# Kernel optimization log

Hardware: AMD Instinct MI355X
Metric: run time of the kernel (lower is better)

## Reference

```python
import jax, jax.numpy as jnp
import numpy as np

B, S, D, H, DFF = 4, 1024, 1024, 16, 4096
MAX_LEN = 1024
DK = D // H
EPS = 1e-5


def _ln(x, g, b):
    m = jnp.mean(x, axis=-1, keepdims=True)
    v = jnp.mean(jnp.square(x - m), axis=-1, keepdims=True)
    return (x - m) / jnp.sqrt(v + EPS) * g + b


def setup_inputs() -> dict:
    key = jax.random.key(0)
    ks = jax.random.split(key, 16)
    s = 0.02
    inp = {
        "x": jax.random.normal(ks[0], (B, S, D), jnp.float32),
        "wq": jax.random.normal(ks[1], (D, D), jnp.float32) * s,
        "bq": jnp.zeros((D,), jnp.float32),
        "wk": jax.random.normal(ks[2], (D, D), jnp.float32) * s,
        "bk": jnp.zeros((D,), jnp.float32),
        "wv": jax.random.normal(ks[3], (D, D), jnp.float32) * s,
        "bv": jnp.zeros((D,), jnp.float32),
        "wo": jax.random.normal(ks[4], (D, D), jnp.float32) * s,
        "bo": jnp.zeros((D,), jnp.float32),
        "rel_table": jax.random.normal(ks[5], (2 * MAX_LEN - 1, H), jnp.float32) * s,
        "ln1_g": jnp.ones((D,), jnp.float32),
        "ln1_b": jnp.zeros((D,), jnp.float32),
        "w1": jax.random.normal(ks[6], (D, DFF), jnp.float32) * s,
        "b1": jnp.zeros((DFF,), jnp.float32),
        "w2": jax.random.normal(ks[7], (DFF, D), jnp.float32) * s,
        "b2": jnp.zeros((D,), jnp.float32),
        "ln2_g": jnp.ones((D,), jnp.float32),
        "ln2_b": jnp.zeros((D,), jnp.float32),
        "mask": jnp.ones((B, 1, 1, S), jnp.int32),
    }
    return inp


def reference(x, wq, bq, wk, bk, wv, bv, wo, bo, rel_table,
              ln1_g, ln1_b, w1, b1, w2, b2, ln2_g, ln2_b, mask):
    # --- multi-head attention with relative position bias (post-LN encoder layer, eval mode) ---
    q = (x @ wq + bq).reshape(B, S, H, DK).transpose(0, 2, 1, 3)  # [B,H,S,dk]
    k = (x @ wk + bk).reshape(B, S, H, DK).transpose(0, 2, 1, 3)
    v = (x @ wv + bv).reshape(B, S, H, DK).transpose(0, 2, 1, 3)

    scores = jnp.einsum('bhqd,bhkd->bhqk', q, k) / jnp.sqrt(jnp.float32(DK))

    # relative position bias: table[(q - k + max_len - 1).clip] -> [1,H,S,S]
    coords = jnp.arange(S)[:, None] - jnp.arange(S)[None, :] + (MAX_LEN - 1)
    coords = jnp.clip(coords, 0, 2 * MAX_LEN - 2)
    bias = rel_table[coords]              # [S,S,H]
    scores = scores + bias.transpose(2, 0, 1)[None]

    scores = jnp.where(mask == 0, jnp.float32(-1e9), scores)
    attn = jax.nn.softmax(scores, axis=-1)
    ctx = jnp.einsum('bhqk,bhkd->bhqd', attn, v)
    ctx = ctx.transpose(0, 2, 1, 3).reshape(B, S, D)
    attn_out = ctx @ wo + bo

    x1 = _ln(x + attn_out, ln1_g, ln1_b)

    ff = jax.nn.relu(x1 @ w1 + b1) @ w2 + b2
    return _ln(x1 + ff, ln2_g, ln2_b)
```

## Files before the change

kernel.cpp:

```cpp
#include <hip/hip_runtime.h>
#include <hip/hip_bf16.h>

typedef __hip_bfloat16 bf16;
typedef __attribute__((ext_vector_type(8))) short short8;
typedef __attribute__((ext_vector_type(4))) float f32x4;

#define LOG2E 1.4426950408889634f

typedef const __attribute__((address_space(1))) void* gptr_t;
typedef __attribute__((address_space(3))) void* sptr_t;

__device__ __forceinline__ void async16(void* lds, const void* g) {
  __builtin_amdgcn_global_load_lds((gptr_t)g, (sptr_t)lds, 16, 0, 0);
}

__device__ __forceinline__ float bf2f(unsigned short u) {
  union { unsigned int i; float f; } c; c.i = ((unsigned int)u) << 16; return c.f;
}


__global__ __launch_bounds__(256) void prep_all(
    const float* __restrict__ x, const float* __restrict__ bq,
    const float* __restrict__ bk, const float* __restrict__ bv,
    const float* __restrict__ wq, const float* __restrict__ wk,
    const float* __restrict__ wv, const float* __restrict__ wo,
    const float* __restrict__ w1, const float* __restrict__ w2,
    bf16* __restrict__ xb, float* __restrict__ bqkv,
    bf16* __restrict__ dqkv, bf16* __restrict__ dwo,
    bf16* __restrict__ dw1, bf16* __restrict__ dw2) {
  const int bid = blockIdx.x;
  if (bid < 4096) {
    int i = (bid * 256 + threadIdx.x) * 4;
    float4 v = *(const float4*)(x + i);
    bf16 h4[4] = {__float2bfloat16(v.x), __float2bfloat16(v.y),
                  __float2bfloat16(v.z), __float2bfloat16(v.w)};
    *(uint2*)((unsigned short*)xb + i) = *(uint2*)h4;
    return;
  }
  if (bid == 16384) {
#pragma unroll
    for (int j = 0; j < 12; ++j) {
      int i = j * 256 + threadIdx.x;
      bqkv[i] = (i < 1024) ? bq[i] : (i < 2048 ? bk[i - 1024] : bv[i - 2048]);
    }
    return;
  }
  __shared__ float tl[32][33];
  const int tid = bid - 4096;
  const float* s;
  bf16* d;
  int NN, KK, n0, k0;
  if (tid < 4096) {
    int m = tid >> 10, tile = tid & 1023;
    s = m == 0 ? wq : m == 1 ? wk : m == 2 ? wv : wo;
    d = m < 3 ? dqkv + (size_t)m * 1024 * 1024 : dwo;
    NN = 1024; KK = 1024;
    n0 = (tile & 31) * 32; k0 = (tile >> 5) * 32;
  } else if (tid < 8192) {
    int tile = tid - 4096;
    s = w1; d = dw1; NN = 4096; KK = 1024;
    n0 = (tile & 127) * 32; k0 = (tile >> 7) * 32;
  } else {
    int tile = tid - 8192;
    s = w2; d = dw2; NN = 1024; KK = 4096;
    n0 = (tile & 31) * 32; k0 = (tile >> 5) * 32;
  }
  const int tx = threadIdx.x & 31, ty = threadIdx.x >> 5;
#pragma unroll
  for (int j = 0; j < 4; ++j)
    tl[ty + j * 8][tx] = s[(size_t)(k0 + ty + j * 8) * NN + n0 + tx];
  __syncthreads();
#pragma unroll
  for (int j = 0; j < 4; ++j)
    d[(size_t)(n0 + ty + j * 8) * KK + k0 + tx] =
        __float2bfloat16(tl[tx][ty + j * 8]);
}


template <int RELU, int VT>
__global__ __launch_bounds__(256) void gemm_bt(
    const bf16* __restrict__ A, const bf16* __restrict__ Bt,
    const float* __restrict__ bias, bf16* __restrict__ C,
    bf16* __restrict__ vt, int M, int N, int K) {
  __shared__ bf16 As[2][128 * 64];
  __shared__ bf16 Bs[2][128 * 64];
  const int t = threadIdx.x;
  const int w = t >> 6, l = t & 63;
  const int m0 = blockIdx.x * 128, n0 = blockIdx.y * 128;
  const int wr = (w >> 1) * 64, wc = (w & 1) * 64;
  const int srow = l >> 3, scol = l & 7;
  const int lm = l & 15, lq = l >> 4;

  f32x4 acc[4][4];
#pragma unroll
  for (int i = 0; i < 4; ++i)
#pragma unroll
    for (int j = 0; j < 4; ++j) acc[i][j] = (f32x4){0.f, 0.f, 0.f, 0.f};

  auto stage = [&](int k0, int d) {
#pragma unroll
    for (int p = 0; p < 4; ++p) {
      int row = p * 32 + w * 8 + srow;
      int gc = scol ^ (row & 7);
      async16(&As[d][(p * 32 + w * 8) * 64], A + (size_t)(m0 + row) * K + k0 + gc * 8);
      async16(&Bs[d][(p * 32 + w * 8) * 64], Bt + (size_t)(n0 + row) * K + k0 + gc * 8);
    }
  };

  stage(0, 0);
  const int niter = K >> 6;
  for (int it = 0; it < niter; ++it) {
    const int d = it & 1;
    __syncthreads();
    short8 af[2][4], bfr[2][4];
#pragma unroll
    for (int kk = 0; kk < 2; ++kk)
#pragma unroll
      for (int mi = 0; mi < 4; ++mi) {
        int rowa = wr + mi * 16 + lm;
        af[kk][mi] = *(const short8*)&As[d][rowa * 64 + (((kk * 4 + lq) ^ (rowa & 7)) << 3)];
        int rowb = wc + mi * 16 + lm;
        bfr[kk][mi] = *(const short8*)&Bs[d][rowb * 64 + (((kk * 4 + lq) ^ (rowb & 7)) << 3)];
      }
    if (it + 1 < niter) stage((it + 1) << 6, d ^ 1);
#pragma unroll
    for (int kk = 0; kk < 2; ++kk)
#pragma unroll
      for (int mi = 0; mi < 4; ++mi)
#pragma unroll
        for (int ni = 0; ni < 4; ++ni)
          acc[mi][ni] = __builtin_amdgcn_mfma_f32_16x16x32_bf16(
              af[kk][mi], bfr[kk][ni], acc[mi][ni], 0, 0, 0);
  }

#pragma unroll
  for (int mi = 0; mi < 4; ++mi)
#pragma unroll
    for (int ni = 0; ni < 4; ++ni) {
      int col = n0 + wc + ni * 16 + lm;
      int row0 = m0 + wr + mi * 16 + lq * 4;
      float bv = bias[col];
      float v[4];
#pragma unroll
      for (int r = 0; r < 4; ++r) {
        v[r] = acc[mi][ni][r] + bv;
        if (RELU) v[r] = fmaxf(v[r], 0.f);
        C[(size_t)(row0 + r) * N + col] = __float2bfloat16(v[r]);
      }
      if (VT && col >= 2048) {
        int vcol = col - 2048;
        int bh = (row0 >> 10) * 16 + (vcol >> 6);
        int dk = vcol & 63;
        int s = row0 & 1023;
        bf16 h4[4] = {__float2bfloat16(v[0]), __float2bfloat16(v[1]),
                      __float2bfloat16(v[2]), __float2bfloat16(v[3])};
        *(uint2*)&vt[((size_t)bh * 64 + dk) * 1024 + s] = *(uint2*)h4;
      }
    }
}

__global__ __launch_bounds__(256) void gemm_bt_splitk(
    const bf16* __restrict__ A, const bf16* __restrict__ Bt,
    bf16* __restrict__ P, int M, int N, int lda, int KS) {
  __shared__ bf16 As[2][128 * 64];
  __shared__ bf16 Bs[2][128 * 64];
  const int t = threadIdx.x;
  const int w = t >> 6, l = t & 63;
  const int m0 = blockIdx.x * 128, n0 = blockIdx.y * 128;
  const int kstart = blockIdx.z * KS;
  const int wr = (w >> 1) * 64, wc = (w & 1) * 64;
  const int srow = l >> 3, scol = l & 7;
  const int lm = l & 15, lq = l >> 4;

  f32x4 acc[4][4];
#pragma unroll
  for (int i = 0; i < 4; ++i)
#pragma unroll
    for (int j = 0; j < 4; ++j) acc[i][j] = (f32x4){0.f, 0.f, 0.f, 0.f};

  auto stage = [&](int k0, int d) {
#pragma unroll
    for (int p = 0; p < 4; ++p) {
      int row = p * 32 + w * 8 + srow;
      int gc = scol ^ (row & 7);
      async16(&As[d][(p * 32 + w * 8) * 64], A + (size_t)(m0 + row) * lda + k0 + gc * 8);
      async16(&Bs[d][(p * 32 + w * 8) * 64], Bt + (size_t)(n0 + row) * lda + k0 + gc * 8);
    }
  };

  stage(kstart, 0);
  const int niter = KS >> 6;
  for (int it = 0; it < niter; ++it) {
    const int d = it & 1;
    __syncthreads();
    short8 af[2][4], bfr[2][4];
#pragma unroll
    for (int kk = 0; kk < 2; ++kk)
#pragma unroll
      for (int mi = 0; mi < 4; ++mi) {
        int rowa = wr + mi * 16 + lm;
        af[kk][mi] = *(const short8*)&As[d][rowa * 64 + (((kk * 4 + lq) ^ (rowa & 7)) << 3)];
        int rowb = wc + mi * 16 + lm;
        bfr[kk][mi] = *(const short8*)&Bs[d][rowb * 64 + (((kk * 4 + lq) ^ (rowb & 7)) << 3)];
      }
    if (it + 1 < niter) stage(kstart + ((it + 1) << 6), d ^ 1);
#pragma unroll
    for (int kk = 0; kk < 2; ++kk)
#pragma unroll
      for (int mi = 0; mi < 4; ++mi)
#pragma unroll
        for (int ni = 0; ni < 4; ++ni)
          acc[mi][ni] = __builtin_amdgcn_mfma_f32_16x16x32_bf16(
              af[kk][mi], bfr[kk][ni], acc[mi][ni], 0, 0, 0);
  }
  bf16* Pz = P + (size_t)blockIdx.z * M * N;
#pragma unroll
  for (int mi = 0; mi < 4; ++mi)
#pragma unroll
    for (int r = 0; r < 4; ++r) {
      int row = m0 + wr + mi * 16 + lq * 4 + r;
#pragma unroll
      for (int ni = 0; ni < 4; ++ni) {
        int col = n0 + wc + ni * 16 + lm;
        Pz[(size_t)row * N + col] = __float2bfloat16(acc[mi][ni][r]);
      }
    }
}


__global__ __launch_bounds__(512, 4) void flash_attn(
    const bf16* __restrict__ qkv, const bf16* __restrict__ vt,
    const float* __restrict__ rel, const int* __restrict__ mask,
    bf16* __restrict__ ctx) {
  __shared__ bf16 Kl[2][64 * 64];
  __shared__ bf16 Vl[2][64 * 64];
  __shared__ bf16 Pl[128 * 64];
  __shared__ float bias_s[2][192];
  __shared__ float mask_s[2][64];

  const int t = threadIdx.x;
  const int w = t >> 6, l = t & 63;
  const int lm = l & 15, lq = l >> 4;
  const int qt = blockIdx.x, bh = blockIdx.y;
  const int b = bh >> 4, h = bh & 15;
  const int q0 = qt * 128;
  const int srow = l >> 3;
  const int gc = (l & 7) ^ srow;
  const int qq = w * 16 + lm;

  auto stage = [&](int d, int k0n) {
    async16(&Kl[d][w * 8 * 64],
            qkv + (size_t)(b * 1024 + k0n + w * 8 + srow) * 3072 + 1024 + h * 64 + gc * 8);
    async16(&Vl[d][w * 8 * 64],
            vt + ((size_t)bh * 64 + w * 8 + srow) * 1024 + k0n + gc * 8);
    if (t < 191) bias_s[d][t] = rel[(q0 - k0n + 960 + t) * 16 + h] * LOG2E;
    if (t < 64) mask_s[d][t] = (mask[b * 1024 + k0n + t] == 0) ? -1.44e9f : 0.f;
  };

#pragma unroll
  for (int p = 0; p < 2; ++p)
    async16(&Pl[(p * 64 + w * 8) * 64],
            qkv + (size_t)(b * 1024 + q0 + p * 64 + w * 8 + srow) * 3072 + h * 64 + gc * 8);
  stage(0, 0);
  __syncthreads();

  short8 qf[2];
#pragma unroll
  for (int kk = 0; kk < 2; ++kk)
    qf[kk] = *(const short8*)&Pl[qq * 64 + (((kk * 4 + lq) ^ (lm & 7)) << 3)];
  __syncthreads();

  float l_acc = 0.f;
  f32x4 acc_o[4];
#pragma unroll
  for (int j = 0; j < 4; ++j) acc_o[j] = (f32x4){0.f, 0.f, 0.f, 0.f};

  const float C0 = 0.125f * LOG2E;

  for (int kt = 0; kt < 16; ++kt) {
    const int d = kt & 1;
    if (kt < 15) stage(d ^ 1, (kt + 1) * 64);

    f32x4 sa[4];
#pragma unroll
    for (int i = 0; i < 4; ++i) sa[i] = (f32x4){0.f, 0.f, 0.f, 0.f};
#pragma unroll
    for (int kk = 0; kk < 2; ++kk) {
      short8 ak[4];
#pragma unroll
      for (int mi = 0; mi < 4; ++mi) {
        int row = mi * 16 + lm;
        ak[mi] = *(const short8*)&Kl[d][row * 64 + (((kk * 4 + lq) ^ (lm & 7)) << 3)];
      }
#pragma unroll
      for (int mi = 0; mi < 4; ++mi)
        sa[mi] = __builtin_amdgcn_mfma_f32_16x16x32_bf16(ak[mi], qf[kk], sa[mi], 0, 0, 0);
    }

    float m4[4][4];
#pragma unroll
    for (int mi = 0; mi < 4; ++mi)
      *(float4*)m4[mi] = *(const float4*)&mask_s[d][mi * 16 + lq * 4];
#pragma unroll
    for (int mi = 0; mi < 4; ++mi)
#pragma unroll
      for (int r = 0; r < 4; ++r) {
        int kl = mi * 16 + lq * 4 + r;
        float p = __builtin_amdgcn_exp2f(
            fmaf(sa[mi][r], C0, bias_s[d][qq - kl + 63] + m4[mi][r]));
        sa[mi][r] = p;
        l_acc += p;
      }

#pragma unroll
    for (int mi = 0; mi < 4; ++mi) {
      bf16 h4[4];
#pragma unroll
      for (int r = 0; r < 4; ++r) h4[r] = __float2bfloat16(sa[mi][r]);
      int chunk = mi * 2 + (lq >> 1);
      *(uint2*)&Pl[qq * 64 + ((chunk ^ (lm & 7)) << 3) + ((lq & 1) << 2)] =
          *(uint2*)h4;
    }

#pragma unroll
    for (int kk2 = 0; kk2 < 2; ++kk2) {
      short8 pf = *(const short8*)&Pl[qq * 64 + (((kk2 * 4 + lq) ^ (lm & 7)) << 3)];
      short8 vf[4];
#pragma unroll
      for (int ni = 0; ni < 4; ++ni) {
        int rowv = ni * 16 + lm;
        vf[ni] = *(const short8*)&Vl[d][rowv * 64 + (((kk2 * 4 + lq) ^ (lm & 7)) << 3)];
      }
#pragma unroll
      for (int ni = 0; ni < 4; ++ni)
        acc_o[ni] = __builtin_amdgcn_mfma_f32_16x16x32_bf16(pf, vf[ni], acc_o[ni], 0, 0, 0);
    }
    __syncthreads();
  }

  l_acc += __shfl_xor(l_acc, 16);
  l_acc += __shfl_xor(l_acc, 32);
  float linv = 1.f / l_acc;
#pragma unroll
  for (int r = 0; r < 4; ++r) {
    float il = __shfl(linv, lq * 4 + r);
    int qx = w * 16 + lq * 4 + r;
    size_t rowbase = (size_t)(b * 1024 + q0 + qx) * 1024 + h * 64;
#pragma unroll
    for (int ni = 0; ni < 4; ++ni)
      ctx[rowbase + ni * 16 + lm] = __float2bfloat16(acc_o[ni][r] * il);
  }
}


template <int NS>
__global__ __launch_bounds__(256) void ln_resid(
    const float* __restrict__ xin, const bf16* __restrict__ part,
    const float* __restrict__ bias,
    const float* __restrict__ gw, const float* __restrict__ bw,
    float* __restrict__ outf, bf16* __restrict__ outb) {
  const int row = blockIdx.x, t = threadIdx.x;
  const size_t base = (size_t)row * 1024 + t * 4;
  float4 xv = *(const float4*)(xin + base);
  float4 bi = *(const float4*)(bias + t * 4);
  float v0 = xv.x + bi.x, v1 = xv.y + bi.y, v2 = xv.z + bi.z, v3 = xv.w + bi.w;
#pragma unroll
  for (int s = 0; s < NS; ++s) {
    const bf16* p = part + (size_t)s * 4194304 + base;
    ushort4 pv = *(const ushort4*)p;
    v0 += bf2f(pv.x); v1 += bf2f(pv.y); v2 += bf2f(pv.z); v3 += bf2f(pv.w);
  }
  float s1 = v0 + v1 + v2 + v3;
  float s2 = v0 * v0 + v1 * v1 + v2 * v2 + v3 * v3;
#pragma unroll
  for (int o = 1; o < 64; o <<= 1) {
    s1 += __shfl_xor(s1, o);
    s2 += __shfl_xor(s2, o);
  }
  __shared__ float red[8];
  const int w = t >> 6, l = t & 63;
  if (l == 0) { red[w] = s1; red[4 + w] = s2; }
  __syncthreads();
  float S1 = red[0] + red[1] + red[2] + red[3];
  float S2 = red[4] + red[5] + red[6] + red[7];
  float mean = S1 * (1.f / 1024.f);
  float var = S2 * (1.f / 1024.f) - mean * mean;
  float rstd = rsqrtf(var + 1e-5f);
  float4 gv = *(const float4*)(gw + t * 4);
  float4 bv = *(const float4*)(bw + t * 4);
  float o0 = (v0 - mean) * rstd * gv.x + bv.x;
  float o1 = (v1 - mean) * rstd * gv.y + bv.y;
  float o2 = (v2 - mean) * rstd * gv.z + bv.z;
  float o3 = (v3 - mean) * rstd * gv.w + bv.w;
  if (outf) {
    float4 ov = {o0, o1, o2, o3};
    *(float4*)(outf + base) = ov;
  }
  if (outb) {
    bf16 h4[4] = {__float2bfloat16(o0), __float2bfloat16(o1),
                  __float2bfloat16(o2), __float2bfloat16(o3)};
    *(uint2*)((unsigned short*)outb + base) = *(uint2*)h4;
  }
}


extern "C" void kernel_launch(void* const* d_in, const int* in_sizes, int n_in,
                              void* d_out, int out_size, void* d_ws, size_t ws_size,
                              hipStream_t stream) {
  (void)in_sizes; (void)n_in; (void)out_size; (void)ws_size;
  const float* x   = (const float*)d_in[0];
  const float* wq  = (const float*)d_in[1];
  const float* bq  = (const float*)d_in[2];
  const float* wk  = (const float*)d_in[3];
  const float* bk  = (const float*)d_in[4];
  const float* wv  = (const float*)d_in[5];
  const float* bv  = (const float*)d_in[6];
  const float* wo  = (const float*)d_in[7];
  const float* bo  = (const float*)d_in[8];
  const float* rel = (const float*)d_in[9];
  const float* g1  = (const float*)d_in[10];
  const float* be1 = (const float*)d_in[11];
  const float* w1  = (const float*)d_in[12];
  const float* b1  = (const float*)d_in[13];
  const float* w2  = (const float*)d_in[14];
  const float* b2  = (const float*)d_in[15];
  const float* g2  = (const float*)d_in[16];
  const float* be2 = (const float*)d_in[17];
  const int* mask  = (const int*)d_in[18];
  float* out = (float*)d_out;

  char* ws = (char*)d_ws;
  bf16*  xb      = (bf16*)(ws + 0);
  bf16*  wqkv_t  = (bf16*)(ws + 8388608);
  bf16*  wo_t    = (bf16*)(ws + 14680064);
  bf16*  w1_t    = (bf16*)(ws + 16777216);
  bf16*  ctx_b   = (bf16*)(ws + 25165824);
  bf16*  x1b     = (bf16*)(ws + 33554432);
  bf16*  qkv_b   = (bf16*)(ws + 41943040);
  bf16*  vtb     = (bf16*)(ws + 67108864);
  bf16*  part_wo = (bf16*)(ws + 41943040);
  bf16*  h1      = (bf16*)(ws + 41943040);
  bf16*  part_ff = (bf16*)(ws + 0);
  bf16*  w2_t    = (bf16*)(ws + 75497472);
  float* x1f     = (float*)(ws + 83886080);
  float* bqkv    = (float*)(ws + 100663296);

  prep_all<<<16385, 256, 0, stream>>>(x, bq, bk, bv, wq, wk, wv, wo, w1, w2,
                                      xb, bqkv, wqkv_t, wo_t, w1_t, w2_t);

  gemm_bt<0, 1><<<dim3(32, 24), 256, 0, stream>>>(
      xb, wqkv_t, bqkv, qkv_b, vtb, 4096, 3072, 1024);
  flash_attn<<<dim3(8, 64), 512, 0, stream>>>(qkv_b, vtb, rel, mask, ctx_b);
  gemm_bt_splitk<<<dim3(32, 8, 2), 256, 0, stream>>>(
      ctx_b, wo_t, part_wo, 4096, 1024, 1024, 512);
  ln_resid<2><<<4096, 256, 0, stream>>>(x, part_wo, bo, g1, be1, x1f, x1b);
  gemm_bt<1, 0><<<dim3(32, 32), 256, 0, stream>>>(
      x1b, w1_t, b1, h1, nullptr, 4096, 4096, 1024);
  gemm_bt_splitk<<<dim3(32, 8, 2), 256, 0, stream>>>(
      h1, w2_t, part_ff, 4096, 1024, 4096, 2048);
  ln_resid<2><<<4096, 256, 0, stream>>>(x1f, part_ff, b2, g2, be2, out, nullptr);
}
```

Baseline: 323.2 us.

## Halve flash-attention query tile and read bf16 residual in second LayerNorm

The attention kernel now uses 64-query tiles with 256 threads per block, doubling the grid to 16x64 blocks. Each wave loads two 8-row chunks of K and V, and the bias and Q staging buffers shrink to match. Separately, the second residual LayerNorm reads the bf16 copy of x1 instead of a separate fp32 copy, so the fp32 x1 write and its re-read are gone. In exchange, the smaller tile loads each K/V tile for fewer queries, so K/V traffic per query goes up, and using a bf16 residual lowers precision.

```diff
diff --git a/kernel.cpp b/kernel.cpp
--- a/kernel.cpp
+++ b/kernel.cpp
@@ -228,14 +228,14 @@
 }
 
 
-__global__ __launch_bounds__(512, 4) void flash_attn(
+__global__ __launch_bounds__(256, 3) void flash_attn(
     const bf16* __restrict__ qkv, const bf16* __restrict__ vt,
     const float* __restrict__ rel, const int* __restrict__ mask,
     bf16* __restrict__ ctx) {
   __shared__ bf16 Kl[2][64 * 64];
   __shared__ bf16 Vl[2][64 * 64];
-  __shared__ bf16 Pl[128 * 64];
-  __shared__ float bias_s[2][192];
+  __shared__ bf16 Pl[64 * 64];
+  __shared__ float bias_s[2][128];
   __shared__ float mask_s[2][64];
 
   const int t = threadIdx.x;
@@ -243,24 +243,30 @@
   const int lm = l & 15, lq = l >> 4;
   const int qt = blockIdx.x, bh = blockIdx.y;
   const int b = bh >> 4, h = bh & 15;
-  const int q0 = qt * 128;
+  const int q0 = qt * 64;
   const int srow = l >> 3;
   const int gc = (l & 7) ^ srow;
   const int qq = w * 16 + lm;
 
   auto stage = [&](int d, int k0n) {
-    async16(&Kl[d][w * 8 * 64],
-            qkv + (size_t)(b * 1024 + k0n + w * 8 + srow) * 3072 + 1024 + h * 64 + gc * 8);
-    async16(&Vl[d][w * 8 * 64],
-            vt + ((size_t)bh * 64 + w * 8 + srow) * 1024 + k0n + gc * 8);
-    if (t < 191) bias_s[d][t] = rel[(q0 - k0n + 960 + t) * 16 + h] * LOG2E;
+#pragma unroll
+    for (int p = 0; p < 2; ++p) {
+      int rbase = w * 16 + p * 8;
+      async16(&Kl[d][rbase * 64],
+              qkv + (size_t)(b * 1024 + k0n + rbase + srow) * 3072 + 1024 + h * 64 + gc * 8);
+      async16(&Vl[d][rbase * 64],
+              vt + ((size_t)bh * 64 + rbase + srow) * 1024 + k0n + gc * 8);
+    }
+    if (t < 127) bias_s[d][t] = rel[(q0 - k0n + 960 + t) * 16 + h] * LOG2E;
     if (t < 64) mask_s[d][t] = (mask[b * 1024 + k0n + t] == 0) ? -1.44e9f : 0.f;
   };
 
 #pragma unroll
-  for (int p = 0; p < 2; ++p)
-    async16(&Pl[(p * 64 + w * 8) * 64],
-            qkv + (size_t)(b * 1024 + q0 + p * 64 + w * 8 + srow) * 3072 + h * 64 + gc * 8);
+  for (int p = 0; p < 2; ++p) {
+    int rbase = w * 16 + p * 8;
+    async16(&Pl[rbase * 64],
+            qkv + (size_t)(b * 1024 + q0 + rbase + srow) * 3072 + h * 64 + gc * 8);
+  }
   stage(0, 0);
   __syncthreads();
 
@@ -353,17 +359,24 @@
 }
 
 
-template <int NS>
+template <typename RT, int NS>
 __global__ __launch_bounds__(256) void ln_resid(
-    const float* __restrict__ xin, const bf16* __restrict__ part,
+    const RT* __restrict__ xin, const bf16* __restrict__ part,
     const float* __restrict__ bias,
     const float* __restrict__ gw, const float* __restrict__ bw,
     float* __restrict__ outf, bf16* __restrict__ outb) {
   const int row = blockIdx.x, t = threadIdx.x;
   const size_t base = (size_t)row * 1024 + t * 4;
-  float4 xv = *(const float4*)(xin + base);
+  float v0, v1, v2, v3;
+  if constexpr (sizeof(RT) == 4) {
+    float4 xv = *(const float4*)(xin + base);
+    v0 = xv.x; v1 = xv.y; v2 = xv.z; v3 = xv.w;
+  } else {
+    ushort4 xv = *(const ushort4*)((const unsigned short*)xin + base);
+    v0 = bf2f(xv.x); v1 = bf2f(xv.y); v2 = bf2f(xv.z); v3 = bf2f(xv.w);
+  }
   float4 bi = *(const float4*)(bias + t * 4);
-  float v0 = xv.x + bi.x, v1 = xv.y + bi.y, v2 = xv.z + bi.z, v3 = xv.w + bi.w;
+  v0 += bi.x; v1 += bi.y; v2 += bi.z; v3 += bi.w;
 #pragma unroll
   for (int s = 0; s < NS; ++s) {
     const bf16* p = part + (size_t)s * 4194304 + base;
@@ -442,7 +455,6 @@
   bf16*  h1      = (bf16*)(ws + 41943040);
   bf16*  part_ff = (bf16*)(ws + 0);
   bf16*  w2_t    = (bf16*)(ws + 75497472);
-  float* x1f     = (float*)(ws + 83886080);
   float* bqkv    = (float*)(ws + 100663296);
 
   prep_all<<<16385, 256, 0, stream>>>(x, bq, bk, bv, wq, wk, wv, wo, w1, w2,
@@ -450,13 +462,13 @@
 
   gemm_bt<0, 1><<<dim3(32, 24), 256, 0, stream>>>(
       xb, wqkv_t, bqkv, qkv_b, vtb, 4096, 3072, 1024);
-  flash_attn<<<dim3(8, 64), 512, 0, stream>>>(qkv_b, vtb, rel, mask, ctx_b);
+  flash_attn<<<dim3(16, 64), 256, 0, stream>>>(qkv_b, vtb, rel, mask, ctx_b);
   gemm_bt_splitk<<<dim3(32, 8, 2), 256, 0, stream>>>(
       ctx_b, wo_t, part_wo, 4096, 1024, 1024, 512);
-  ln_resid<2><<<4096, 256, 0, stream>>>(x, part_wo, bo, g1, be1, x1f, x1b);
+  ln_resid<float, 2><<<4096, 256, 0, stream>>>(x, part_wo, bo, g1, be1, nullptr, x1b);
   gemm_bt<1, 0><<<dim3(32, 32), 256, 0, stream>>>(
       x1b, w1_t, b1, h1, nullptr, 4096, 4096, 1024);
   gemm_bt_splitk<<<dim3(32, 8, 2), 256, 0, stream>>>(
       h1, w2_t, part_ff, 4096, 1024, 4096, 2048);
-  ln_resid<2><<<4096, 256, 0, stream>>>(x1f, part_ff, b2, g2, be2, out, nullptr);
-}
+  ln_resid<bf16, 2><<<4096, 256, 0, stream>>>(x1b, part_ff, b2, g2, be2, out, nullptr);
+}
```

Result: no change. 319.7 us (-1.1%).

## Split attention over two key halves with combine kernel; feed bf16 residual to LN2

Applied to the files above, without the earlier changes.

The flash attention grid gains a z dimension that splits the 16 key tiles into two halves. Each half writes an unnormalized bf16 context partial and its row sums, and a new combine kernel adds the partials and normalizes. This doubles the block count so more of the GPU is busy during attention, at the cost of an extra kernel launch and a round trip of partial results through memory. Separately, the final LayerNorm now reads the bf16 copy of x1 instead of an fp32 copy, which removes one fp32 write and read but lowers the precision of the residual.

```diff
diff --git a/kernel.cpp b/kernel.cpp
--- a/kernel.cpp
+++ b/kernel.cpp
@@ -231,7 +231,7 @@
 __global__ __launch_bounds__(512, 4) void flash_attn(
     const bf16* __restrict__ qkv, const bf16* __restrict__ vt,
     const float* __restrict__ rel, const int* __restrict__ mask,
-    bf16* __restrict__ ctx) {
+    bf16* __restrict__ ctx_part, float* __restrict__ lpart) {
   __shared__ bf16 Kl[2][64 * 64];
   __shared__ bf16 Vl[2][64 * 64];
   __shared__ bf16 Pl[128 * 64];
@@ -241,9 +241,10 @@
   const int t = threadIdx.x;
   const int w = t >> 6, l = t & 63;
   const int lm = l & 15, lq = l >> 4;
-  const int qt = blockIdx.x, bh = blockIdx.y;
+  const int qt = blockIdx.x, bh = blockIdx.y, z = blockIdx.z;
   const int b = bh >> 4, h = bh & 15;
   const int q0 = qt * 128;
+  const int kt0 = z * 8;
   const int srow = l >> 3;
   const int gc = (l & 7) ^ srow;
   const int qq = w * 16 + lm;
@@ -261,7 +262,7 @@
   for (int p = 0; p < 2; ++p)
     async16(&Pl[(p * 64 + w * 8) * 64],
             qkv + (size_t)(b * 1024 + q0 + p * 64 + w * 8 + srow) * 3072 + h * 64 + gc * 8);
-  stage(0, 0);
+  stage(0, kt0 * 64);
   __syncthreads();
 
   short8 qf[2];
@@ -277,9 +278,9 @@
 
   const float C0 = 0.125f * LOG2E;
 
-  for (int kt = 0; kt < 16; ++kt) {
+  for (int kt = kt0; kt < kt0 + 8; ++kt) {
     const int d = kt & 1;
-    if (kt < 15) stage(d ^ 1, (kt + 1) * 64);
+    if (kt + 1 < kt0 + 8) stage(d ^ 1, (kt + 1) * 64);
 
     f32x4 sa[4];
 #pragma unroll
@@ -340,30 +341,57 @@
 
   l_acc += __shfl_xor(l_acc, 16);
   l_acc += __shfl_xor(l_acc, 32);
-  float linv = 1.f / l_acc;
+  if (lq == 0)
+    lpart[(size_t)z * 65536 + (size_t)bh * 1024 + q0 + qq] = l_acc;
+  bf16* cp = ctx_part + (size_t)z * 4194304;
 #pragma unroll
   for (int r = 0; r < 4; ++r) {
-    float il = __shfl(linv, lq * 4 + r);
     int qx = w * 16 + lq * 4 + r;
     size_t rowbase = (size_t)(b * 1024 + q0 + qx) * 1024 + h * 64;
 #pragma unroll
     for (int ni = 0; ni < 4; ++ni)
-      ctx[rowbase + ni * 16 + lm] = __float2bfloat16(acc_o[ni][r] * il);
-  }
-}
-
-
-template <int NS>
+      cp[rowbase + ni * 16 + lm] = __float2bfloat16(acc_o[ni][r]);
+  }
+}
+
+__global__ __launch_bounds__(256) void combine_ctx(
+    const bf16* __restrict__ part, const float* __restrict__ lpart,
+    bf16* __restrict__ ctx) {
+  const int row = blockIdx.x, t = threadIdx.x;
+  const size_t base = (size_t)row * 1024 + t * 4;
+  const int b = row >> 10, s = row & 1023;
+  const int h = t >> 4;
+  float lsum = lpart[(size_t)(b * 16 + h) * 1024 + s] +
+               lpart[65536 + (size_t)(b * 16 + h) * 1024 + s];
+  float inv = 1.f / lsum;
+  ushort4 p0 = *(const ushort4*)((const unsigned short*)part + base);
+  ushort4 p1 = *(const ushort4*)((const unsigned short*)part + 4194304 + base);
+  bf16 h4[4] = {__float2bfloat16((bf2f(p0.x) + bf2f(p1.x)) * inv),
+                __float2bfloat16((bf2f(p0.y) + bf2f(p1.y)) * inv),
+                __float2bfloat16((bf2f(p0.z) + bf2f(p1.z)) * inv),
+                __float2bfloat16((bf2f(p0.w) + bf2f(p1.w)) * inv)};
+  *(uint2*)((unsigned short*)ctx + base) = *(uint2*)h4;
+}
+
+
+template <typename RT, int NS>
 __global__ __launch_bounds__(256) void ln_resid(
-    const float* __restrict__ xin, const bf16* __restrict__ part,
+    const RT* __restrict__ xin, const bf16* __restrict__ part,
     const float* __restrict__ bias,
     const float* __restrict__ gw, const float* __restrict__ bw,
     float* __restrict__ outf, bf16* __restrict__ outb) {
   const int row = blockIdx.x, t = threadIdx.x;
   const size_t base = (size_t)row * 1024 + t * 4;
-  float4 xv = *(const float4*)(xin + base);
+  float v0, v1, v2, v3;
+  if constexpr (sizeof(RT) == 4) {
+    float4 xv = *(const float4*)(xin + base);
+    v0 = xv.x; v1 = xv.y; v2 = xv.z; v3 = xv.w;
+  } else {
+    ushort4 xv = *(const ushort4*)((const unsigned short*)xin + base);
+    v0 = bf2f(xv.x); v1 = bf2f(xv.y); v2 = bf2f(xv.z); v3 = bf2f(xv.w);
+  }
   float4 bi = *(const float4*)(bias + t * 4);
-  float v0 = xv.x + bi.x, v1 = xv.y + bi.y, v2 = xv.z + bi.z, v3 = xv.w + bi.w;
+  v0 += bi.x; v1 += bi.y; v2 += bi.z; v3 += bi.w;
 #pragma unroll
   for (int s = 0; s < NS; ++s) {
     const bf16* p = part + (size_t)s * 4194304 + base;
@@ -430,33 +458,36 @@
   float* out = (float*)d_out;
 
   char* ws = (char*)d_ws;
-  bf16*  xb      = (bf16*)(ws + 0);
-  bf16*  wqkv_t  = (bf16*)(ws + 8388608);
-  bf16*  wo_t    = (bf16*)(ws + 14680064);
-  bf16*  w1_t    = (bf16*)(ws + 16777216);
-  bf16*  ctx_b   = (bf16*)(ws + 25165824);
-  bf16*  x1b     = (bf16*)(ws + 33554432);
-  bf16*  qkv_b   = (bf16*)(ws + 41943040);
-  bf16*  vtb     = (bf16*)(ws + 67108864);
-  bf16*  part_wo = (bf16*)(ws + 41943040);
-  bf16*  h1      = (bf16*)(ws + 41943040);
-  bf16*  part_ff = (bf16*)(ws + 0);
-  bf16*  w2_t    = (bf16*)(ws + 75497472);
-  float* x1f     = (float*)(ws + 83886080);
-  float* bqkv    = (float*)(ws + 100663296);
+  bf16*  xb       = (bf16*)(ws + 0);
+  bf16*  wqkv_t   = (bf16*)(ws + 8388608);
+  bf16*  wo_t     = (bf16*)(ws + 14680064);
+  bf16*  w1_t     = (bf16*)(ws + 16777216);
+  bf16*  ctx_b    = (bf16*)(ws + 25165824);
+  bf16*  x1b      = (bf16*)(ws + 33554432);
+  float* lpart    = (float*)(ws + 33554432);
+  bf16*  qkv_b    = (bf16*)(ws + 41943040);
+  bf16*  vtb      = (bf16*)(ws + 67108864);
+  bf16*  part_wo  = (bf16*)(ws + 41943040);
+  bf16*  h1       = (bf16*)(ws + 41943040);
+  bf16*  part_ff  = (bf16*)(ws + 0);
+  bf16*  w2_t     = (bf16*)(ws + 75497472);
+  bf16*  ctx_part = (bf16*)(ws + 83886080);
+  float* bqkv     = (float*)(ws + 100663296);
 
   prep_all<<<16385, 256, 0, stream>>>(x, bq, bk, bv, wq, wk, wv, wo, w1, w2,
                                       xb, bqkv, wqkv_t, wo_t, w1_t, w2_t);
 
   gemm_bt<0, 1><<<dim3(32, 24), 256, 0, stream>>>(
       xb, wqkv_t, bqkv, qkv_b, vtb, 4096, 3072, 1024);
-  flash_attn<<<dim3(8, 64), 512, 0, stream>>>(qkv_b, vtb, rel, mask, ctx_b);
+  flash_attn<<<dim3(8, 64, 2), 512, 0, stream>>>(
+      qkv_b, vtb, rel, mask, ctx_part, lpart);
+  combine_ctx<<<4096, 256, 0, stream>>>(ctx_part, lpart, ctx_b);
   gemm_bt_splitk<<<dim3(32, 8, 2), 256, 0, stream>>>(
       ctx_b, wo_t, part_wo, 4096, 1024, 1024, 512);
-  ln_resid<2><<<4096, 256, 0, stream>>>(x, part_wo, bo, g1, be1, x1f, x1b);
+  ln_resid<float, 2><<<4096, 256, 0, stream>>>(x, part_wo, bo, g1, be1, nullptr, x1b);
   gemm_bt<1, 0><<<dim3(32, 32), 256, 0, stream>>>(
       x1b, w1_t, b1, h1, nullptr, 4096, 4096, 1024);
   gemm_bt_splitk<<<dim3(32, 8, 2), 256, 0, stream>>>(
       h1, w2_t, part_ff, 4096, 1024, 4096, 2048);
-  ln_resid<2><<<4096, 256, 0, stream>>>(x1f, part_ff, b2, g2, be2, out, nullptr);
-}
+  ln_resid<bf16, 2><<<4096, 256, 0, stream>>>(x1b, part_ff, b2, g2, be2, out, nullptr);
+}
```

Measured after the change: 316.2 us. 1.02x faster.
